# Optimization experiments

Measured on AMD Instinct MI355X. Metric: run time of the kernel, lower is better.

Reference implementation:

```python
import jax, jax.numpy as jnp
import numpy as np

NPOINT = 1024
BRANCHES = [(0.4, 32), (0.8, 64)]  # (radius, nsample)
SPECS = [[67, 64, 64, 128], [67, 64, 128, 256]]  # mlp specs after use_xyz (+3)
EPS = 1e-5


def setup_inputs() -> dict:
    key = jax.random.key(0)
    ks = jax.random.split(key, 16)
    B, N, C = 8, 8192, 64
    inp = {
        "xyz": jax.random.normal(ks[0], (B, N, 3), jnp.float32),
        "features": jax.random.normal(ks[1], (B, C, N), jnp.float32),
    }
    ki = 2
    for bi, spec in enumerate(SPECS):
        for li in range(3):
            o, i = spec[li + 1], spec[li]
            inp[f"w{bi}_{li}"] = jax.random.normal(ks[ki], (o, i), jnp.float32) * (1.0 / np.sqrt(i)); ki += 1
            inp[f"g{bi}_{li}"] = jnp.ones((o,), jnp.float32)
            inp[f"b{bi}_{li}"] = jnp.zeros((o,), jnp.float32)
    return inp


def fps(pts, npoint):
    # pts: [B, N+1, 3] (mean point prepended); sequential farthest point sampling
    B, N1, _ = pts.shape

    def step(carry, _):
        dist, far = carry
        idx3 = jnp.broadcast_to(far[:, None, None], (B, 1, 3))
        centroid = jnp.take_along_axis(pts, idx3, axis=1)  # [B,1,3]
        d = jnp.sum((pts - centroid) ** 2, axis=-1)        # [B,N+1]
        dist = jnp.minimum(dist, d)
        far2 = jnp.argmax(dist, axis=-1)
        return (dist, far2), centroid[:, 0, :]

    dist0 = jnp.full((B, N1), 1e10, jnp.float32)
    far0 = jnp.zeros((B,), jnp.int32)
    _, locs = jax.lax.scan(step, (dist0, far0), None, length=npoint)
    return jnp.transpose(locs, (1, 0, 2))  # [B, npoint, 3]


def ball_query(xyz, new_xyz, radius, nsample):
    # first <=nsample indices with dist^2 < radius^2, padded with first valid (0 if none)
    B, N, _ = xyz.shape
    d2 = jnp.sum((new_xyz[:, :, None, :] - xyz[:, None, :, :]) ** 2, axis=-1)  # [B,S,N]
    score = jnp.where(d2 < radius * radius, jnp.arange(N, dtype=jnp.int32), N)
    vals, _ = jax.lax.top_k(-score, nsample)  # smallest scores = earliest valid indices
    idx = -vals                               # [B,S,nsample], N marks invalid
    first = idx[..., :1]
    first = jnp.where(first < N, first, 0)
    return jnp.where(idx < N, idx, first)


def _forward(xyz, features, params):
    mean = jnp.mean(xyz, axis=1, keepdims=True)
    pts = jnp.concatenate([mean, xyz], axis=1)          # prepend mean point
    new_xyz = jax.lax.stop_gradient(fps(pts, NPOINT))   # [B,npoint,3] (torch no_grad)
    outs = []
    for (radius, nsample), layers in zip(BRANCHES, params):
        idx = ball_query(xyz, new_xyz, radius, nsample)           # [B,S,K]
        gxyz = jax.vmap(lambda p, i: p[i])(xyz, idx)              # [B,S,K,3]
        rel = jnp.transpose(gxyz - new_xyz[:, :, None, :], (0, 3, 1, 2))  # [B,3,S,K]
        gfeat = jax.vmap(lambda f, i: f[:, i])(features, idx)     # [B,C,S,K]
        x = jnp.concatenate([rel, gfeat], axis=1)                 # [B,3+C,S,K]
        for W, g, b in layers:  # Conv2d 1x1 (no bias) + BatchNorm (train stats) + ReLU
            x = jnp.einsum('oi,bisk->bosk', W, x)
            m = jnp.mean(x, axis=(0, 2, 3), keepdims=True)
            v = jnp.var(x, axis=(0, 2, 3), keepdims=True)
            x = (x - m) / jnp.sqrt(v + EPS) * g[None, :, None, None] + b[None, :, None, None]
            x = jax.nn.relu(x)
        outs.append(jnp.max(x, axis=3))                           # [B,Cout,S]
    return new_xyz, jnp.concatenate(outs, axis=1)


def reference(xyz, features,
              w0_0, g0_0, b0_0, w0_1, g0_1, b0_1, w0_2, g0_2, b0_2,
              w1_0, g1_0, b1_0, w1_1, g1_1, b1_1, w1_2, g1_2, b1_2):
    params = [
        [(w0_0, g0_0, b0_0), (w0_1, g0_1, b0_1), (w0_2, g0_2, b0_2)],
        [(w1_0, g1_0, b1_0), (w1_1, g1_1, b1_1), (w1_2, g1_2, b1_2)],
    ]
    return _forward(xyz, features, params)
```

## Files before the change

kernel.cpp:

```cpp
#include <hip/hip_runtime.h>
#include <hip/hip_bf16.h>
#include <cstdint>


typedef __attribute__((ext_vector_type(8))) short short8;
typedef __attribute__((ext_vector_type(4))) float f32x4;
typedef __attribute__((ext_vector_type(2))) float f32x2;

__device__ __forceinline__ float bf2f(unsigned short u) {
    return __uint_as_float(((unsigned)u) << 16);
}
__device__ __forceinline__ unsigned short f2bf(float f) {
    unsigned u = __float_as_uint(f);
    return (unsigned short)((u + 0x7fffu + ((u >> 16) & 1u)) >> 16);
}

__device__ __forceinline__ float wave_red_max_f32(float v) {
#define DPPSTEP(ctrl)                                                                  \
    {                                                                                  \
        int _t = __builtin_amdgcn_update_dpp((int)0xFF800000, __float_as_int(v), ctrl, \
                                             0xf, 0xf, false);                         \
        v = fmaxf(v, __int_as_float(_t));                                              \
    }
    DPPSTEP(0x111) DPPSTEP(0x112) DPPSTEP(0x114) DPPSTEP(0x118) DPPSTEP(0x142) DPPSTEP(0x143)
#undef DPPSTEP
    return v;
}
__device__ __forceinline__ unsigned wave_red_min_u32(unsigned v) {
#define DPPSTEP(ctrl)                                                                   \
    {                                                                                   \
        unsigned _t = (unsigned)__builtin_amdgcn_update_dpp((int)0xFFFFFFFF, (int)v,    \
                                                            ctrl, 0xf, 0xf, false);     \
        v = v < _t ? v : _t;                                                            \
    }
    DPPSTEP(0x111) DPPSTEP(0x112) DPPSTEP(0x114) DPPSTEP(0x118) DPPSTEP(0x142) DPPSTEP(0x143)
#undef DPPSTEP
    return v;
}
__device__ __forceinline__ unsigned long long u64max(unsigned long long a, unsigned long long b) {
    return a > b ? a : b;
}
__device__ __forceinline__ unsigned u32min(unsigned a, unsigned b) { return a < b ? a : b; }

static const size_t OFF_WBF   = 0;
static const size_t OFF_STATS = 262144;
static const size_t STATS_BYTES = 720896;
static const size_t OFF_AFF   = 1048576;
static const size_t OFF_IDX0  = 2097152;
static const size_t OFF_IDX1  = 3145728;
static const size_t OFF_MX    = 5242880;
static const size_t OFF_MN    = 13631488;
static const size_t OFF_Y0    = 22020096;
static const size_t OFF_Y1    = 90177536;
static const size_t OFF_FEATT = 211812352;

__global__ __launch_bounds__(512) void fused_pre(
    const float* __restrict__ xyz, const float* __restrict__ feat,
    float* __restrict__ newxyz, unsigned short* __restrict__ ft,
    const float* __restrict__ w0, const float* __restrict__ w1, const float* __restrict__ w2,
    const float* __restrict__ w3, const float* __restrict__ w4, const float* __restrict__ w5,
    unsigned short* __restrict__ wb) {
    __shared__ union alignas(16) SM {
        struct {
            float ptsx[8200], ptsy[8200], ptsz[8200];
            float ldsM[16][3];
            float meanv[3];
            unsigned long long sKey[2][8];
            float cbuf[3072];
        } f;
        float tile[64][65];
    } sm;
    const int tid = threadIdx.x;

    if (blockIdx.x >= 1032) {
        int id = (int)(blockIdx.x - 1032) * 512 + tid;
        const int psz[6] = {6144, 4096, 8192, 6144, 8192, 32768};
        const int Kp[6] = {96, 64, 64, 96, 64, 128};
        const int Ks[6] = {67, 64, 64, 67, 64, 128};
        const float* wp[6] = {w0, w1, w2, w3, w4, w5};
        int off = 0;
        for (int l = 0; l < 6; ++l) {
            if (id < off + psz[l]) {
                int e = id - off;
                int m = e / Kp[l], k = e - m * Kp[l];
                float v = (k < Ks[l]) ? wp[l][m * Ks[l] + k] : 0.f;
                wb[id] = f2bf(v);
                return;
            }
            off += psz[l];
        }
        return;
    }

    if (blockIdx.x >= 8) {
        int tb = (int)blockIdx.x - 8;
        int b = tb >> 7;
        int j0 = (tb & 127) * 64;
#pragma unroll
        for (int i = 0; i < 8; ++i) {
            int e = i * 512 + tid;
            int c = e >> 6, j = e & 63;
            sm.tile[j][c] = feat[((size_t)b * 64 + c) * 8192 + j0 + j];
        }
        __syncthreads();
#pragma unroll
        for (int i = 0; i < 8; ++i) {
            int e = i * 512 + tid;
            int j = e >> 6, c = e & 63;
            ft[((size_t)(b * 8192 + j0 + j)) * 96 + 3 + c] = f2bf(sm.tile[j][c]);
        }
        if (tid < 64) {
            int j = tid;
            size_t base = ((size_t)(b * 8192 + j0 + j)) * 96;
            const float* xp = xyz + ((size_t)b * 8192 + j0 + j) * 3;
            ft[base + 0] = f2bf(xp[0]);
            ft[base + 1] = f2bf(xp[1]);
            ft[base + 2] = f2bf(xp[2]);
        } else if (tid < 128) {
            int j = tid - 64;
            size_t base = ((size_t)(b * 8192 + j0 + j)) * 96;
            for (int c = 67; c < 96; ++c) ft[base + c] = 0;
        }
        return;
    }

    const int b = blockIdx.x;
    const int t = tid;
    const int lane = t & 63, wv = t >> 6;
    const float* xb = xyz + (size_t)b * 8192 * 3;

    f32x2 px[8], py[8], pz[8], d[8];
#pragma unroll
    for (int k = 0; k < 8; ++k) {
        int q0 = t + 512 * (2 * k);
        int q1 = t + 512 * (2 * k + 1);
        px[k].x = xb[q0 * 3 + 0]; px[k].y = xb[q1 * 3 + 0];
        py[k].x = xb[q0 * 3 + 1]; py[k].y = xb[q1 * 3 + 1];
        pz[k].x = xb[q0 * 3 + 2]; pz[k].y = xb[q1 * 3 + 2];
        d[k].x = 1e10f; d[k].y = 1e10f;
        sm.f.ptsx[q0 + 1] = px[k].x; sm.f.ptsx[q1 + 1] = px[k].y;
        sm.f.ptsy[q0 + 1] = py[k].x; sm.f.ptsy[q1 + 1] = py[k].y;
        sm.f.ptsz[q0 + 1] = pz[k].x; sm.f.ptsz[q1 + 1] = pz[k].y;
    }
    float sxA = 0.f, syA = 0.f, szA = 0.f;
    float sxB = 0.f, syB = 0.f, szB = 0.f;
    int uA = (t + 1023) & 1023;
    int uB = (t + 511) & 1023;
#pragma unroll
    for (int j = 0; j < 8; ++j) {
        int ia = uA + 1024 * j;
        int ib = uB + 1024 * j;
        sxA += xb[ia * 3 + 0]; syA += xb[ia * 3 + 1]; szA += xb[ia * 3 + 2];
        sxB += xb[ib * 3 + 0]; syB += xb[ib * 3 + 1]; szB += xb[ib * 3 + 2];
    }
#pragma unroll
    for (int off = 32; off; off >>= 1) {
        sxA += __shfl_xor(sxA, off, 64);
        syA += __shfl_xor(syA, off, 64);
        szA += __shfl_xor(szA, off, 64);
        sxB += __shfl_xor(sxB, off, 64);
        syB += __shfl_xor(syB, off, 64);
        szB += __shfl_xor(szB, off, 64);
    }
    if (lane == 0) {
        sm.f.ldsM[wv][0] = sxA; sm.f.ldsM[wv][1] = syA; sm.f.ldsM[wv][2] = szA;
        sm.f.ldsM[wv + 8][0] = sxB; sm.f.ldsM[wv + 8][1] = syB; sm.f.ldsM[wv + 8][2] = szB;
    }
    __syncthreads();
    if (t < 3) {
        float s = 0.f;
        for (int w = 0; w < 16; ++w) s += sm.f.ldsM[w][t];
        sm.f.meanv[t] = s * (1.f / 8192.f);
    }
    __syncthreads();
    float cx = sm.f.meanv[0], cy = sm.f.meanv[1], cz = sm.f.meanv[2];
    const float mmx = cx, mmy = cy, mmz = cz;
    float dm = 1e10f;
    if (t == 0) { sm.f.ptsx[0] = cx; sm.f.ptsy[0] = cy; sm.f.ptsz[0] = cz; }
    __syncthreads();

    for (int it = 0; it < 1024; ++it) {
        if (t == 0) {
            sm.f.cbuf[it * 3 + 0] = cx;
            sm.f.cbuf[it * 3 + 1] = cy;
            sm.f.cbuf[it * 3 + 2] = cz;
        }
        f32x2 c0, c1, c2, vm2;
        c0.x = cx; c0.y = cx; c1.x = cy; c1.y = cy; c2.x = cz; c2.y = cz;
        vm2.x = -1e30f; vm2.y = -1e30f;
        {
#pragma clang fp contract(off)
#pragma unroll
            for (int k = 0; k < 8; ++k) {
                f32x2 dx = px[k] - c0;
                f32x2 dy = py[k] - c1;
                f32x2 dz = pz[k] - c2;
                f32x2 dd = (dx * dx + dy * dy) + dz * dz;
                f32x2 nd = __builtin_elementwise_min(d[k], dd);
                d[k] = nd;
                vm2 = __builtin_elementwise_max(vm2, nd);
            }
        }
        float vmax = fmaxf(vm2.x, vm2.y);
        if (t == 0) {
            float dx = __fsub_rn(mmx, cx);
            float dy = __fsub_rn(mmy, cy);
            float dz = __fsub_rn(mmz, cz);
            float dd = __fadd_rn(__fadd_rn(__fmul_rn(dx, dx), __fmul_rn(dy, dy)), __fmul_rn(dz, dz));
            dm = fminf(dm, dd);
            vmax = fmaxf(vmax, dm);
        }
        float wm = wave_red_max_f32(vmax);
        float bmaxw = __int_as_float(__builtin_amdgcn_readlane(__float_as_int(wm), 63));
        unsigned m2[8];
#pragma unroll
        for (int k = 0; k < 8; ++k) {
            unsigned i0 = (d[k].x == bmaxw) ? (unsigned)(t + 512 * (2 * k) + 1) : 0xFFFFFFFFu;
            unsigned i1 = (d[k].y == bmaxw) ? (unsigned)(t + 512 * (2 * k + 1) + 1) : 0xFFFFFFFFu;
            m2[k] = u32min(i0, i1);
        }
        unsigned n0 = u32min(m2[0], m2[1]), n1 = u32min(m2[2], m2[3]);
        unsigned n2 = u32min(m2[4], m2[5]), n3 = u32min(m2[6], m2[7]);
        unsigned mi = u32min(u32min(n0, n1), u32min(n2, n3));
        if (t == 0 && dm == bmaxw) mi = 0u;
        unsigned wmin = wave_red_min_u32(mi);
        unsigned miw = (unsigned)__builtin_amdgcn_readlane((int)wmin, 63);
        int par = it & 1;
        if (lane == 0)
            sm.f.sKey[par][wv] = ((unsigned long long)__float_as_uint(bmaxw) << 32) |
                                 (unsigned long long)(8192u - miw);
        __syncthreads();
        unsigned long long ka[8];
#pragma unroll
        for (int i = 0; i < 8; ++i) ka[i] = sm.f.sKey[par][i];
        unsigned long long p0 = u64max(ka[0], ka[1]), p1 = u64max(ka[2], ka[3]);
        unsigned long long p2 = u64max(ka[4], ka[5]), p3 = u64max(ka[6], ka[7]);
        unsigned long long kk = u64max(u64max(p0, p1), u64max(p2, p3));
        int far = 8192 - (int)(unsigned)(kk & 0xffffffffull);
        cx = sm.f.ptsx[far];
        cy = sm.f.ptsy[far];
        cz = sm.f.ptsz[far];
    }
    __syncthreads();
    float* ob = newxyz + (size_t)b * 3072;
#pragma unroll
    for (int i = 0; i < 6; ++i) ob[t + 512 * i] = sm.f.cbuf[t + 512 * i];
}

__global__ void ball_query2(const float* __restrict__ xyz, const float* __restrict__ newxyz,
                            int* __restrict__ idx0, int* __restrict__ idx1) {
    int bid = blockIdx.x;
    int br = (bid >= 2048);
    int K = br ? 64 : 32;
    float r2 = br ? (0.8f * 0.8f) : (0.4f * 0.4f);
    int* idxout = br ? idx1 : idx0;
    int wid = (((bid & 2047) * 256) + threadIdx.x) >> 6;
    int lane = threadIdx.x & 63;
    int b = wid >> 10;
    const float* q = newxyz + (size_t)wid * 3;
    float qx = q[0], qy = q[1], qz = q[2];
    const float* xb = xyz + (size_t)b * 8192 * 3;
    int* out = idxout + (size_t)wid * K;
    int count = 0;
    int first = 0;
    for (int base = 0; base < 8192 && count < K; base += 64) {
        int j = base + lane;
        float dx = __fsub_rn(xb[j * 3 + 0], qx);
        float dy = __fsub_rn(xb[j * 3 + 1], qy);
        float dz = __fsub_rn(xb[j * 3 + 2], qz);
        float d2 = __fadd_rn(__fadd_rn(__fmul_rn(dx, dx), __fmul_rn(dy, dy)), __fmul_rn(dz, dz));
        bool in = d2 < r2;
        unsigned long long m = __ballot(in);
        if (count == 0 && m) first = base + __ffsll((long long)m) - 1;
        if (in) {
            int pos = count + __popcll(m & ((1ull << lane) - 1ull));
            if (pos < K) out[pos] = j;
        }
        count += __popcll(m);
    }
    if (count < K) {
        int fillv = (count > 0) ? first : 0;
        for (int p = count + lane; p < K; p += 64) out[p] = fillv;
    }
}

template <int Mp, int Kp, int IN_MODE, int OUT_MODE, int KSH>
__global__ __launch_bounds__(256) void gemm_mfma(
    const unsigned short* __restrict__ Wb, const unsigned short* __restrict__ Xin,
    const float* __restrict__ aff, const int* __restrict__ idx,
    const unsigned short* __restrict__ ftp, const float* __restrict__ newxyz,
    unsigned short* __restrict__ Yout, float* __restrict__ MX, float* __restrict__ MN,
    float* __restrict__ statS, float* __restrict__ statQ) {
    constexpr int MT = Mp / 64;
    constexpr int KS = Kp / 32;
    __shared__ unsigned short Bs[256 * KS * 8];
    __shared__ float sAux[256];
    int* sAuxI = (int*)sAux;

    const int tid = threadIdx.x;
    const int w = tid >> 6;
    const int lane = tid & 63;
    const int n = lane & 15;
    const int quad = lane >> 4;
    const int rbase = w * (Mp / 4);
    const long col0 = (long)blockIdx.x * 64;

    short8 a[MT][KS];
#pragma unroll
    for (int mt = 0; mt < MT; ++mt)
#pragma unroll
        for (int ks = 0; ks < KS; ++ks)
            a[mt][ks] = *(const short8*)(Wb + (size_t)(rbase + mt * 16 + n) * Kp + ks * 32 + quad * 8);

    if constexpr (IN_MODE == 0) {
        if (tid < 64) {
            long colg = col0 + tid;
            sAuxI[tid] = idx[colg];
            long sk = colg >> KSH;
            sAux[64 + tid] = newxyz[sk * 3 + 0];
            sAux[128 + tid] = newxyz[sk * 3 + 1];
            sAux[192 + tid] = newxyz[sk * 3 + 2];
        }
    } else {
        if (tid < 2 * Kp) sAux[tid] = aff[tid];
    }
    __syncthreads();

#pragma unroll
    for (int i = 0; i < KS; ++i) {
        int p = i * 256 + tid;
        int pl = p & 63;
        int pn = pl & 15;
        int pq = pl >> 4;
        int rest = p >> 6;
        int pks = rest % KS;
        int pnt = rest / KS;
        int col = pnt * 16 + pn;
        int kc = pks * 4 + pq;
        short8 v;
        if constexpr (IN_MODE == 0) {
            const int bb = (int)(col0 >> (KSH + 10));
            int j = sAuxI[col];
            v = *(const short8*)(ftp + ((long)(bb * 8192 + j)) * 96 + kc * 8);
            if (kc == 0) {
                v[0] = (short)f2bf(bf2f((unsigned short)v[0]) - sAux[64 + col]);
                v[1] = (short)f2bf(bf2f((unsigned short)v[1]) - sAux[128 + col]);
                v[2] = (short)f2bf(bf2f((unsigned short)v[2]) - sAux[192 + col]);
            }
        } else {
            short8 raw = *(const short8*)(Xin + (col0 + col) * (long)Kp + kc * 8);
#pragma unroll
            for (int e = 0; e < 8; ++e) {
                float xf = bf2f((unsigned short)raw[e]);
                xf = fmaxf(fmaf(xf, sAux[kc * 8 + e], sAux[Kp + kc * 8 + e]), 0.f);
                v[e] = (short)f2bf(xf);
            }
        }
        *(short8*)(&Bs[p * 8]) = v;
    }
    __syncthreads();

    f32x4 acc[MT][4];
#pragma unroll
    for (int mt = 0; mt < MT; ++mt)
#pragma unroll
        for (int nt = 0; nt < 4; ++nt)
#pragma unroll
            for (int r = 0; r < 4; ++r) acc[mt][nt][r] = 0.f;

#pragma unroll
    for (int ks = 0; ks < KS; ++ks) {
#pragma unroll
        for (int nt = 0; nt < 4; ++nt) {
            short8 bfr = *(const short8*)(&Bs[((nt * KS + ks) * 64 + lane) * 8]);
#pragma unroll
            for (int mt = 0; mt < MT; ++mt)
                acc[mt][nt] = __builtin_amdgcn_mfma_f32_16x16x32_bf16(a[mt][ks], bfr, acc[mt][nt], 0, 0, 0);
        }
    }

    const int slot = (int)(blockIdx.x & 127);
#pragma unroll
    for (int mt = 0; mt < MT; ++mt)
#pragma unroll
        for (int r = 0; r < 4; ++r) {
            float s = 0.f, q = 0.f;
#pragma unroll
            for (int nt = 0; nt < 4; ++nt) {
                float v = acc[mt][nt][r];
                s += v;
                q = fmaf(v, v, q);
            }
#pragma unroll
            for (int off = 1; off < 16; off <<= 1) {
                s += __shfl_xor(s, off, 16);
                q += __shfl_xor(q, off, 16);
            }
            if (n == 0) {
                int ch = rbase + mt * 16 + quad * 4 + r;
                atomicAdd(statS + (size_t)ch * 128 + slot, s);
                atomicAdd(statQ + (size_t)ch * 128 + slot, q);
            }
        }

    if constexpr (OUT_MODE == 0) {
#pragma unroll
        for (int mt = 0; mt < MT; ++mt)
#pragma unroll
            for (int nt = 0; nt < 4; ++nt) {
                long col = col0 + nt * 16 + n;
                unsigned p0 = f2bf(acc[mt][nt][0]) | ((unsigned)f2bf(acc[mt][nt][1]) << 16);
                unsigned p1 = f2bf(acc[mt][nt][2]) | ((unsigned)f2bf(acc[mt][nt][3]) << 16);
                uint2 st; st.x = p0; st.y = p1;
                *(uint2*)(Yout + col * Mp + rbase + mt * 16 + quad * 4) = st;
            }
    } else {
#pragma unroll
        for (int mt = 0; mt < MT; ++mt)
#pragma unroll
            for (int r = 0; r < 4; ++r) {
                if constexpr (KSH == 6) {
                    float mx = acc[mt][0][r], mn = acc[mt][0][r];
#pragma unroll
                    for (int nt = 1; nt < 4; ++nt) {
                        mx = fmaxf(mx, acc[mt][nt][r]);
                        mn = fminf(mn, acc[mt][nt][r]);
                    }
#pragma unroll
                    for (int off = 1; off < 16; off <<= 1) {
                        mx = fmaxf(mx, __shfl_xor(mx, off, 16));
                        mn = fminf(mn, __shfl_xor(mn, off, 16));
                    }
                    if (n == 0) {
                        int ch = rbase + mt * 16 + quad * 4 + r;
                        long g = col0 >> 6;
                        MX[(long)ch * 8192 + g] = mx;
                        MN[(long)ch * 8192 + g] = mn;
                    }
                } else {
#pragma unroll
                    for (int gh = 0; gh < 2; ++gh) {
                        float mx = fmaxf(acc[mt][2 * gh][r], acc[mt][2 * gh + 1][r]);
                        float mn = fminf(acc[mt][2 * gh][r], acc[mt][2 * gh + 1][r]);
#pragma unroll
                        for (int off = 1; off < 16; off <<= 1) {
                            mx = fmaxf(mx, __shfl_xor(mx, off, 16));
                            mn = fminf(mn, __shfl_xor(mn, off, 16));
                        }
                        if (n == 0) {
                            int ch = rbase + mt * 16 + quad * 4 + r;
                            long g = (col0 >> 5) + gh;
                            MX[(long)ch * 8192 + g] = mx;
                            MN[(long)ch * 8192 + g] = mn;
                        }
                    }
                }
            }
    }
}

__global__ void finalize_kernel(const float* __restrict__ sS, const float* __restrict__ sQ,
                                const float* __restrict__ g, const float* __restrict__ b,
                                float* __restrict__ aff, int C, float invCount) {
    int c = threadIdx.x + blockIdx.x * blockDim.x;
    if (c >= C) return;
    float s = 0.f, q = 0.f;
    for (int k = 0; k < 128; ++k) { s += sS[c * 128 + k]; q += sQ[c * 128 + k]; }
    float mean = s * invCount;
    float var = fmaxf(q * invCount - mean * mean, 0.f);
    float sc = g[c] / sqrtf(var + 1e-5f);
    float sh = b[c] - mean * sc;
    aff[c] = sc;
    aff[C + c] = sh;
}

__global__ void final_out_kernel(const float* __restrict__ MX, const float* __restrict__ MN,
                                 const float* __restrict__ aff, float* __restrict__ out1,
                                 int Cout, int cOff) {
    long i = (long)blockIdx.x * 256 + threadIdx.x;
    int c = (int)(i >> 13);
    int gidx = (int)(i & 8191);
    int b = gidx >> 10, s = gidx & 1023;
    float sc = aff[c], sh = aff[Cout + c];
    float v = fmaxf(fmaxf(sc * MX[i] + sh, sc * MN[i] + sh), 0.f);
    out1[((long)b * 384 + cOff + c) * 1024 + s] = v;
}

extern "C" void kernel_launch(void* const* d_in, const int* in_sizes, int n_in,
                              void* d_out, int out_size, void* d_ws, size_t ws_size,
                              hipStream_t stream) {
    const float* xyz = (const float*)d_in[0];
    const float* feat = (const float*)d_in[1];
    const float *W[6], *G[6], *Bi[6];
    for (int l = 0; l < 6; ++l) {
        W[l] = (const float*)d_in[2 + l * 3];
        G[l] = (const float*)d_in[3 + l * 3];
        Bi[l] = (const float*)d_in[4 + l * 3];
    }
    char* ws = (char*)d_ws;
    float* out0 = (float*)d_out;
    float* out1 = (float*)d_out + 24576;

    unsigned short* wb = (unsigned short*)(ws + OFF_WBF);
    float* stats = (float*)(ws + OFF_STATS);
    float* affine = (float*)(ws + OFF_AFF);
    int* idx0 = (int*)(ws + OFF_IDX0);
    int* idx1 = (int*)(ws + OFF_IDX1);
    float* mx = (float*)(ws + OFF_MX);
    float* mn = (float*)(ws + OFF_MN);
    unsigned short* y0 = (unsigned short*)(ws + OFF_Y0);
    unsigned short* y1 = (unsigned short*)(ws + OFF_Y1);
    unsigned short* ftp = (unsigned short*)(ws + OFF_FEATT);

    hipMemsetAsync(stats, 0, STATS_BYTES, stream);
    fused_pre<<<1160, 512, 0, stream>>>(xyz, feat, out0, ftp, W[0], W[1], W[2], W[3], W[4],
                                        W[5], wb);
    ball_query2<<<4096, 256, 0, stream>>>(xyz, out0, idx0, idx1);

    const int wOff[6] = {0, 6144, 10240, 18432, 24576, 32768};
    int stOff[6], afOff[6];
    {
        const int Cs[6] = {64, 64, 128, 64, 128, 256};
        int so = 0, ao = 0;
        for (int l = 0; l < 6; ++l) {
            stOff[l] = so; so += Cs[l] * 256;
            afOff[l] = ao; ao += Cs[l] * 2;
        }
    }

    for (int br = 0; br < 2; ++br) {
        const int K = br ? 64 : 32;
        const long NCOL = 8L * 1024 * K;
        int* idx = br ? idx1 : idx0;
        const int l0 = br * 3, l1 = br * 3 + 1, l2 = br * 3 + 2;
        const int M2 = br ? 256 : 128;
        const float invCount = 1.f / (float)NCOL;
        const int nblk = (int)(NCOL / 64);

        if (br == 0) {
            gemm_mfma<64, 96, 0, 0, 5><<<nblk, 256, 0, stream>>>(
                wb + wOff[l0], nullptr, nullptr, idx, ftp, out0, y0, nullptr, nullptr,
                stats + stOff[l0], stats + stOff[l0] + 64 * 128);
            finalize_kernel<<<1, 256, 0, stream>>>(stats + stOff[l0], stats + stOff[l0] + 64 * 128,
                                                   G[l0], Bi[l0], affine + afOff[l0], 64, invCount);
            gemm_mfma<64, 64, 1, 0, 5><<<nblk, 256, 0, stream>>>(
                wb + wOff[l1], y0, affine + afOff[l0], nullptr, nullptr, nullptr, y1, nullptr,
                nullptr, stats + stOff[l1], stats + stOff[l1] + 64 * 128);
            finalize_kernel<<<1, 256, 0, stream>>>(stats + stOff[l1], stats + stOff[l1] + 64 * 128,
                                                   G[l1], Bi[l1], affine + afOff[l1], 64, invCount);
            gemm_mfma<128, 64, 1, 1, 5><<<nblk, 256, 0, stream>>>(
                wb + wOff[l2], y1, affine + afOff[l1], nullptr, nullptr, nullptr, nullptr, mx, mn,
                stats + stOff[l2], stats + stOff[l2] + 128 * 128);
            finalize_kernel<<<1, 256, 0, stream>>>(stats + stOff[l2], stats + stOff[l2] + 128 * 128,
                                                   G[l2], Bi[l2], affine + afOff[l2], 128, invCount);
        } else {
            gemm_mfma<64, 96, 0, 0, 6><<<nblk, 256, 0, stream>>>(
                wb + wOff[l0], nullptr, nullptr, idx, ftp, out0, y0, nullptr, nullptr,
                stats + stOff[l0], stats + stOff[l0] + 64 * 128);
            finalize_kernel<<<1, 256, 0, stream>>>(stats + stOff[l0], stats + stOff[l0] + 64 * 128,
                                                   G[l0], Bi[l0], affine + afOff[l0], 64, invCount);
            gemm_mfma<128, 64, 1, 0, 6><<<nblk, 256, 0, stream>>>(
                wb + wOff[l1], y0, affine + afOff[l0], nullptr, nullptr, nullptr, y1, nullptr,
                nullptr, stats + stOff[l1], stats + stOff[l1] + 128 * 128);
            finalize_kernel<<<1, 256, 0, stream>>>(stats + stOff[l1], stats + stOff[l1] + 128 * 128,
                                                   G[l1], Bi[l1], affine + afOff[l1], 128, invCount);
            gemm_mfma<256, 128, 1, 1, 6><<<nblk, 256, 0, stream>>>(
                wb + wOff[l2], y1, affine + afOff[l1], nullptr, nullptr, nullptr, nullptr, mx, mn,
                stats + stOff[l2], stats + stOff[l2] + 256 * 128);
            finalize_kernel<<<1, 256, 0, stream>>>(stats + stOff[l2], stats + stOff[l2] + 256 * 128,
                                                   G[l2], Bi[l2], affine + afOff[l2], 256, invCount);
        }

        final_out_kernel<<<(M2 * 8192) / 256, 256, 0, stream>>>(mx, mn, affine + afOff[l2], out1,
                                                                M2, br ? 128 : 0);
    }
}
```

Measured before the change: 1.765 ms.

## Shrink FPS block to 256 threads and widen GEMM column tiles to 128

The farthest-point-sampling block drops from 512 to 256 threads. Each thread now holds 32 points in registers, which cuts the number of waves in the per-iteration cross-wave argmax reduction from 8 to 4. The MFMA GEMM kernels gain an NT template parameter so most layers process 128 columns per block instead of 64, reusing the loaded weight fragments across more columns. The costs are higher register pressure in FPS, more serial work per thread, and larger shared-memory tiles in the GEMM.

```diff
diff --git a/kernel.cpp b/kernel.cpp
--- a/kernel.cpp
+++ b/kernel.cpp
@@ -54,7 +54,7 @@
 static const size_t OFF_Y1    = 90177536;
 static const size_t OFF_FEATT = 211812352;
 
-__global__ __launch_bounds__(512) void fused_pre(
+__global__ __launch_bounds__(256) void fused_pre(
     const float* __restrict__ xyz, const float* __restrict__ feat,
     float* __restrict__ newxyz, unsigned short* __restrict__ ft,
     const float* __restrict__ w0, const float* __restrict__ w1, const float* __restrict__ w2,
@@ -65,7 +65,7 @@
             float ptsx[8200], ptsy[8200], ptsz[8200];
             float ldsM[16][3];
             float meanv[3];
-            unsigned long long sKey[2][8];
+            unsigned long long sKey[2][4];
             float cbuf[3072];
         } f;
         float tile[64][65];
@@ -73,7 +73,7 @@
     const int tid = threadIdx.x;
 
     if (blockIdx.x >= 1032) {
-        int id = (int)(blockIdx.x - 1032) * 512 + tid;
+        int id = (int)(blockIdx.x - 1032) * 256 + tid;
         const int psz[6] = {6144, 4096, 8192, 6144, 8192, 32768};
         const int Kp[6] = {96, 64, 64, 96, 64, 128};
         const int Ks[6] = {67, 64, 64, 67, 64, 128};
@@ -97,15 +97,15 @@
         int b = tb >> 7;
         int j0 = (tb & 127) * 64;
 #pragma unroll
-        for (int i = 0; i < 8; ++i) {
-            int e = i * 512 + tid;
+        for (int i = 0; i < 16; ++i) {
+            int e = i * 256 + tid;
             int c = e >> 6, j = e & 63;
             sm.tile[j][c] = feat[((size_t)b * 64 + c) * 8192 + j0 + j];
         }
         __syncthreads();
 #pragma unroll
-        for (int i = 0; i < 8; ++i) {
-            int e = i * 512 + tid;
+        for (int i = 0; i < 16; ++i) {
+            int e = i * 256 + tid;
             int j = e >> 6, c = e & 63;
             ft[((size_t)(b * 8192 + j0 + j)) * 96 + 3 + c] = f2bf(sm.tile[j][c]);
         }
@@ -129,11 +129,11 @@
     const int lane = t & 63, wv = t >> 6;
     const float* xb = xyz + (size_t)b * 8192 * 3;
 
-    f32x2 px[8], py[8], pz[8], d[8];
-#pragma unroll
-    for (int k = 0; k < 8; ++k) {
-        int q0 = t + 512 * (2 * k);
-        int q1 = t + 512 * (2 * k + 1);
+    f32x2 px[16], py[16], pz[16], d[16];
+#pragma unroll
+    for (int k = 0; k < 16; ++k) {
+        int q0 = t + 256 * (2 * k);
+        int q1 = t + 256 * (2 * k + 1);
         px[k].x = xb[q0 * 3 + 0]; px[k].y = xb[q1 * 3 + 0];
         py[k].x = xb[q0 * 3 + 1]; py[k].y = xb[q1 * 3 + 1];
         pz[k].x = xb[q0 * 3 + 2]; pz[k].y = xb[q1 * 3 + 2];
@@ -142,29 +142,36 @@
         sm.f.ptsy[q0 + 1] = py[k].x; sm.f.ptsy[q1 + 1] = py[k].y;
         sm.f.ptsz[q0 + 1] = pz[k].x; sm.f.ptsz[q1 + 1] = pz[k].y;
     }
-    float sxA = 0.f, syA = 0.f, szA = 0.f;
-    float sxB = 0.f, syB = 0.f, szB = 0.f;
-    int uA = (t + 1023) & 1023;
-    int uB = (t + 511) & 1023;
-#pragma unroll
-    for (int j = 0; j < 8; ++j) {
-        int ia = uA + 1024 * j;
-        int ib = uB + 1024 * j;
-        sxA += xb[ia * 3 + 0]; syA += xb[ia * 3 + 1]; szA += xb[ia * 3 + 2];
-        sxB += xb[ib * 3 + 0]; syB += xb[ib * 3 + 1]; szB += xb[ib * 3 + 2];
-    }
-#pragma unroll
-    for (int off = 32; off; off >>= 1) {
-        sxA += __shfl_xor(sxA, off, 64);
-        syA += __shfl_xor(syA, off, 64);
-        szA += __shfl_xor(szA, off, 64);
-        sxB += __shfl_xor(sxB, off, 64);
-        syB += __shfl_xor(syB, off, 64);
-        szB += __shfl_xor(szB, off, 64);
-    }
-    if (lane == 0) {
-        sm.f.ldsM[wv][0] = sxA; sm.f.ldsM[wv][1] = syA; sm.f.ldsM[wv][2] = szA;
-        sm.f.ldsM[wv + 8][0] = sxB; sm.f.ldsM[wv + 8][1] = syB; sm.f.ldsM[wv + 8][2] = szB;
+    {
+        float sx[4], sy[4], sz[4];
+#pragma unroll
+        for (int m = 0; m < 4; ++m) {
+            int u = (t + 256 * m + 1023) & 1023;
+            float ax = 0.f, ay = 0.f, az = 0.f;
+#pragma unroll
+            for (int jj = 0; jj < 8; ++jj) {
+                int ia = u + 1024 * jj;
+                ax += xb[ia * 3 + 0]; ay += xb[ia * 3 + 1]; az += xb[ia * 3 + 2];
+            }
+            sx[m] = ax; sy[m] = ay; sz[m] = az;
+        }
+#pragma unroll
+        for (int off = 32; off; off >>= 1) {
+#pragma unroll
+            for (int m = 0; m < 4; ++m) {
+                sx[m] += __shfl_xor(sx[m], off, 64);
+                sy[m] += __shfl_xor(sy[m], off, 64);
+                sz[m] += __shfl_xor(sz[m], off, 64);
+            }
+        }
+        if (lane == 0) {
+#pragma unroll
+            for (int m = 0; m < 4; ++m) {
+                sm.f.ldsM[wv + 4 * m][0] = sx[m];
+                sm.f.ldsM[wv + 4 * m][1] = sy[m];
+                sm.f.ldsM[wv + 4 * m][2] = sz[m];
+            }
+        }
     }
     __syncthreads();
     if (t < 3) {
@@ -191,7 +198,7 @@
         {
 #pragma clang fp contract(off)
 #pragma unroll
-            for (int k = 0; k < 8; ++k) {
+            for (int k = 0; k < 16; ++k) {
                 f32x2 dx = px[k] - c0;
                 f32x2 dy = py[k] - c1;
                 f32x2 dz = pz[k] - c2;
@@ -212,16 +219,18 @@
         }
         float wm = wave_red_max_f32(vmax);
         float bmaxw = __int_as_float(__builtin_amdgcn_readlane(__float_as_int(wm), 63));
-        unsigned m2[8];
-#pragma unroll
-        for (int k = 0; k < 8; ++k) {
-            unsigned i0 = (d[k].x == bmaxw) ? (unsigned)(t + 512 * (2 * k) + 1) : 0xFFFFFFFFu;
-            unsigned i1 = (d[k].y == bmaxw) ? (unsigned)(t + 512 * (2 * k + 1) + 1) : 0xFFFFFFFFu;
+        unsigned m2[16];
+#pragma unroll
+        for (int k = 0; k < 16; ++k) {
+            unsigned i0 = (d[k].x == bmaxw) ? (unsigned)(t + 256 * (2 * k) + 1) : 0xFFFFFFFFu;
+            unsigned i1 = (d[k].y == bmaxw) ? (unsigned)(t + 256 * (2 * k + 1) + 1) : 0xFFFFFFFFu;
             m2[k] = u32min(i0, i1);
         }
-        unsigned n0 = u32min(m2[0], m2[1]), n1 = u32min(m2[2], m2[3]);
-        unsigned n2 = u32min(m2[4], m2[5]), n3 = u32min(m2[6], m2[7]);
-        unsigned mi = u32min(u32min(n0, n1), u32min(n2, n3));
+#pragma unroll
+        for (int s = 8; s; s >>= 1)
+#pragma unroll
+            for (int k = 0; k < s; ++k) m2[k] = u32min(m2[k], m2[k + s]);
+        unsigned mi = m2[0];
         if (t == 0 && dm == bmaxw) mi = 0u;
         unsigned wmin = wave_red_min_u32(mi);
         unsigned miw = (unsigned)__builtin_amdgcn_readlane((int)wmin, 63);
@@ -230,12 +239,10 @@
             sm.f.sKey[par][wv] = ((unsigned long long)__float_as_uint(bmaxw) << 32) |
                                  (unsigned long long)(8192u - miw);
         __syncthreads();
-        unsigned long long ka[8];
-#pragma unroll
-        for (int i = 0; i < 8; ++i) ka[i] = sm.f.sKey[par][i];
-        unsigned long long p0 = u64max(ka[0], ka[1]), p1 = u64max(ka[2], ka[3]);
-        unsigned long long p2 = u64max(ka[4], ka[5]), p3 = u64max(ka[6], ka[7]);
-        unsigned long long kk = u64max(u64max(p0, p1), u64max(p2, p3));
+        unsigned long long ka[4];
+#pragma unroll
+        for (int i = 0; i < 4; ++i) ka[i] = sm.f.sKey[par][i];
+        unsigned long long kk = u64max(u64max(ka[0], ka[1]), u64max(ka[2], ka[3]));
         int far = 8192 - (int)(unsigned)(kk & 0xffffffffull);
         cx = sm.f.ptsx[far];
         cy = sm.f.ptsy[far];
@@ -244,7 +251,7 @@
     __syncthreads();
     float* ob = newxyz + (size_t)b * 3072;
 #pragma unroll
-    for (int i = 0; i < 6; ++i) ob[t + 512 * i] = sm.f.cbuf[t + 512 * i];
+    for (int i = 0; i < 12; ++i) ob[t + 256 * i] = sm.f.cbuf[t + 256 * i];
 }
 
 __global__ void ball_query2(const float* __restrict__ xyz, const float* __restrict__ newxyz,
@@ -284,7 +291,7 @@
     }
 }
 
-template <int Mp, int Kp, int IN_MODE, int OUT_MODE, int KSH>
+template <int Mp, int Kp, int IN_MODE, int OUT_MODE, int KSH, int NT>
 __global__ __launch_bounds__(256) void gemm_mfma(
     const unsigned short* __restrict__ Wb, const unsigned short* __restrict__ Xin,
     const float* __restrict__ aff, const int* __restrict__ idx,
@@ -293,8 +300,10 @@
     float* __restrict__ statS, float* __restrict__ statQ) {
     constexpr int MT = Mp / 64;
     constexpr int KS = Kp / 32;
-    __shared__ unsigned short Bs[256 * KS * 8];
-    __shared__ float sAux[256];
+    constexpr int NC = NT * 16;
+    constexpr int NCHUNK = NT * KS * 64;
+    __shared__ unsigned short Bs[NCHUNK * 8];
+    __shared__ float sAux[NT * 64];
     int* sAuxI = (int*)sAux;
 
     const int tid = threadIdx.x;
@@ -303,7 +312,7 @@
     const int n = lane & 15;
     const int quad = lane >> 4;
     const int rbase = w * (Mp / 4);
-    const long col0 = (long)blockIdx.x * 64;
+    const long col0 = (long)blockIdx.x * NC;
 
     short8 a[MT][KS];
 #pragma unroll
@@ -313,13 +322,13 @@
             a[mt][ks] = *(const short8*)(Wb + (size_t)(rbase + mt * 16 + n) * Kp + ks * 32 + quad * 8);
 
     if constexpr (IN_MODE == 0) {
-        if (tid < 64) {
+        if (tid < NC) {
             long colg = col0 + tid;
             sAuxI[tid] = idx[colg];
             long sk = colg >> KSH;
-            sAux[64 + tid] = newxyz[sk * 3 + 0];
-            sAux[128 + tid] = newxyz[sk * 3 + 1];
-            sAux[192 + tid] = newxyz[sk * 3 + 2];
+            sAux[NC + tid] = newxyz[sk * 3 + 0];
+            sAux[2 * NC + tid] = newxyz[sk * 3 + 1];
+            sAux[3 * NC + tid] = newxyz[sk * 3 + 2];
         }
     } else {
         if (tid < 2 * Kp) sAux[tid] = aff[tid];
@@ -327,7 +336,7 @@
     __syncthreads();
 
 #pragma unroll
-    for (int i = 0; i < KS; ++i) {
+    for (int i = 0; i < NCHUNK / 256; ++i) {
         int p = i * 256 + tid;
         int pl = p & 63;
         int pn = pl & 15;
@@ -343,9 +352,9 @@
             int j = sAuxI[col];
             v = *(const short8*)(ftp + ((long)(bb * 8192 + j)) * 96 + kc * 8);
             if (kc == 0) {
-                v[0] = (short)f2bf(bf2f((unsigned short)v[0]) - sAux[64 + col]);
-                v[1] = (short)f2bf(bf2f((unsigned short)v[1]) - sAux[128 + col]);
-                v[2] = (short)f2bf(bf2f((unsigned short)v[2]) - sAux[192 + col]);
+                v[0] = (short)f2bf(bf2f((unsigned short)v[0]) - sAux[NC + col]);
+                v[1] = (short)f2bf(bf2f((unsigned short)v[1]) - sAux[2 * NC + col]);
+                v[2] = (short)f2bf(bf2f((unsigned short)v[2]) - sAux[3 * NC + col]);
             }
         } else {
             short8 raw = *(const short8*)(Xin + (col0 + col) * (long)Kp + kc * 8);
@@ -360,18 +369,18 @@
     }
     __syncthreads();
 
-    f32x4 acc[MT][4];
+    f32x4 acc[MT][NT];
 #pragma unroll
     for (int mt = 0; mt < MT; ++mt)
 #pragma unroll
-        for (int nt = 0; nt < 4; ++nt)
+        for (int nt = 0; nt < NT; ++nt)
 #pragma unroll
             for (int r = 0; r < 4; ++r) acc[mt][nt][r] = 0.f;
 
 #pragma unroll
     for (int ks = 0; ks < KS; ++ks) {
 #pragma unroll
-        for (int nt = 0; nt < 4; ++nt) {
+        for (int nt = 0; nt < NT; ++nt) {
             short8 bfr = *(const short8*)(&Bs[((nt * KS + ks) * 64 + lane) * 8]);
 #pragma unroll
             for (int mt = 0; mt < MT; ++mt)
@@ -386,7 +395,7 @@
         for (int r = 0; r < 4; ++r) {
             float s = 0.f, q = 0.f;
 #pragma unroll
-            for (int nt = 0; nt < 4; ++nt) {
+            for (int nt = 0; nt < NT; ++nt) {
                 float v = acc[mt][nt][r];
                 s += v;
                 q = fmaf(v, v, q);
@@ -407,7 +416,7 @@
 #pragma unroll
         for (int mt = 0; mt < MT; ++mt)
 #pragma unroll
-            for (int nt = 0; nt < 4; ++nt) {
+            for (int nt = 0; nt < NT; ++nt) {
                 long col = col0 + nt * 16 + n;
                 unsigned p0 = f2bf(acc[mt][nt][0]) | ((unsigned)f2bf(acc[mt][nt][1]) << 16);
                 unsigned p1 = f2bf(acc[mt][nt][2]) | ((unsigned)f2bf(acc[mt][nt][3]) << 16);
@@ -415,16 +424,19 @@
                 *(uint2*)(Yout + col * Mp + rbase + mt * 16 + quad * 4) = st;
             }
     } else {
+        constexpr int GRP = (1 << KSH) / 16;
+        constexpr int NG = NT / GRP;
 #pragma unroll
         for (int mt = 0; mt < MT; ++mt)
 #pragma unroll
             for (int r = 0; r < 4; ++r) {
-                if constexpr (KSH == 6) {
-                    float mx = acc[mt][0][r], mn = acc[mt][0][r];
-#pragma unroll
-                    for (int nt = 1; nt < 4; ++nt) {
-                        mx = fmaxf(mx, acc[mt][nt][r]);
-                        mn = fminf(mn, acc[mt][nt][r]);
+#pragma unroll
+                for (int gh = 0; gh < NG; ++gh) {
+                    float mx = acc[mt][GRP * gh][r], mn = acc[mt][GRP * gh][r];
+#pragma unroll
+                    for (int e = 1; e < GRP; ++e) {
+                        mx = fmaxf(mx, acc[mt][GRP * gh + e][r]);
+                        mn = fminf(mn, acc[mt][GRP * gh + e][r]);
                     }
 #pragma unroll
                     for (int off = 1; off < 16; off <<= 1) {
@@ -433,26 +445,9 @@
                     }
                     if (n == 0) {
                         int ch = rbase + mt * 16 + quad * 4 + r;
-                        long g = col0 >> 6;
+                        long g = (col0 >> KSH) + gh;
                         MX[(long)ch * 8192 + g] = mx;
                         MN[(long)ch * 8192 + g] = mn;
-                    }
-                } else {
-#pragma unroll
-                    for (int gh = 0; gh < 2; ++gh) {
-                        float mx = fmaxf(acc[mt][2 * gh][r], acc[mt][2 * gh + 1][r]);
-                        float mn = fminf(acc[mt][2 * gh][r], acc[mt][2 * gh + 1][r]);
-#pragma unroll
-                        for (int off = 1; off < 16; off <<= 1) {
-                            mx = fmaxf(mx, __shfl_xor(mx, off, 16));
-                            mn = fminf(mn, __shfl_xor(mn, off, 16));
-                        }
-                        if (n == 0) {
-                            int ch = rbase + mt * 16 + quad * 4 + r;
-                            long g = (col0 >> 5) + gh;
-                            MX[(long)ch * 8192 + g] = mx;
-                            MN[(long)ch * 8192 + g] = mn;
-                        }
                     }
                 }
             }
@@ -513,7 +508,7 @@
     unsigned short* ftp = (unsigned short*)(ws + OFF_FEATT);
 
     hipMemsetAsync(stats, 0, STATS_BYTES, stream);
-    fused_pre<<<1160, 512, 0, stream>>>(xyz, feat, out0, ftp, W[0], W[1], W[2], W[3], W[4],
+    fused_pre<<<1288, 256, 0, stream>>>(xyz, feat, out0, ftp, W[0], W[1], W[2], W[3], W[4],
                                         W[5], wb);
     ball_query2<<<4096, 256, 0, stream>>>(xyz, out0, idx0, idx1);
 
@@ -535,36 +530,37 @@
         const int l0 = br * 3, l1 = br * 3 + 1, l2 = br * 3 + 2;
         const int M2 = br ? 256 : 128;
         const float invCount = 1.f / (float)NCOL;
-        const int nblk = (int)(NCOL / 64);
+        const int nblk128 = (int)(NCOL / 128);
+        const int nblk64 = (int)(NCOL / 64);
 
         if (br == 0) {
-            gemm_mfma<64, 96, 0, 0, 5><<<nblk, 256, 0, stream>>>(
+            gemm_mfma<64, 96, 0, 0, 5, 8><<<nblk128, 256, 0, stream>>>(
                 wb + wOff[l0], nullptr, nullptr, idx, ftp, out0, y0, nullptr, nullptr,
                 stats + stOff[l0], stats + stOff[l0] + 64 * 128);
             finalize_kernel<<<1, 256, 0, stream>>>(stats + stOff[l0], stats + stOff[l0] + 64 * 128,
                                                    G[l0], Bi[l0], affine + afOff[l0], 64, invCount);
-            gemm_mfma<64, 64, 1, 0, 5><<<nblk, 256, 0, stream>>>(
+            gemm_mfma<64, 64, 1, 0, 5, 8><<<nblk128, 256, 0, stream>>>(
                 wb + wOff[l1], y0, affine + afOff[l0], nullptr, nullptr, nullptr, y1, nullptr,
                 nullptr, stats + stOff[l1], stats + stOff[l1] + 64 * 128);
             finalize_kernel<<<1, 256, 0, stream>>>(stats + stOff[l1], stats + stOff[l1] + 64 * 128,
                                                    G[l1], Bi[l1], affine + afOff[l1], 64, invCount);
-            gemm_mfma<128, 64, 1, 1, 5><<<nblk, 256, 0, stream>>>(
+            gemm_mfma<128, 64, 1, 1, 5, 8><<<nblk128, 256, 0, stream>>>(
                 wb + wOff[l2], y1, affine + afOff[l1], nullptr, nullptr, nullptr, nullptr, mx, mn,
                 stats + stOff[l2], stats + stOff[l2] + 128 * 128);
             finalize_kernel<<<1, 256, 0, stream>>>(stats + stOff[l2], stats + stOff[l2] + 128 * 128,
                                                    G[l2], Bi[l2], affine + afOff[l2], 128, invCount);
         } else {
-            gemm_mfma<64, 96, 0, 0, 6><<<nblk, 256, 0, stream>>>(
+            gemm_mfma<64, 96, 0, 0, 6, 8><<<nblk128, 256, 0, stream>>>(
                 wb + wOff[l0], nullptr, nullptr, idx, ftp, out0, y0, nullptr, nullptr,
                 stats + stOff[l0], stats + stOff[l0] + 64 * 128);
             finalize_kernel<<<1, 256, 0, stream>>>(stats + stOff[l0], stats + stOff[l0] + 64 * 128,
                                                    G[l0], Bi[l0], affine + afOff[l0], 64, invCount);
-            gemm_mfma<128, 64, 1, 0, 6><<<nblk, 256, 0, stream>>>(
+            gemm_mfma<128, 64, 1, 0, 6, 8><<<nblk128, 256, 0, stream>>>(
                 wb + wOff[l1], y0, affine + afOff[l0], nullptr, nullptr, nullptr, y1, nullptr,
                 nullptr, stats + stOff[l1], stats + stOff[l1] + 128 * 128);
             finalize_kernel<<<1, 256, 0, stream>>>(stats + stOff[l1], stats + stOff[l1] + 128 * 128,
                                                    G[l1], Bi[l1], affine + afOff[l1], 128, invCount);
-            gemm_mfma<256, 128, 1, 1, 6><<<nblk, 256, 0, stream>>>(
+            gemm_mfma<256, 128, 1, 1, 6, 4><<<nblk64, 256, 0, stream>>>(
                 wb + wOff[l2], y1, affine + afOff[l1], nullptr, nullptr, nullptr, nullptr, mx, mn,
                 stats + stOff[l2], stats + stOff[l2] + 256 * 128);
             finalize_kernel<<<1, 256, 0, stream>>>(stats + stOff[l2], stats + stOff[l2] + 256 * 128,
```

Measured after the change: 1.637 ms. 1.08x faster.
